# Optimization experiments

Hardware: AMD Instinct MI355X
Metric: run time of the kernel (lower is better)

The kernel has to match this reference:

```python
import jax, jax.numpy as jnp
import numpy as np


def _norm_adj(edge_index, edge_weights, num_nodes):
    """Faithful port of edge_index2norm_adj: dense scatter + self-loops +
    symmetric degree normalization (deg_inv_sqrt is detached in the original)."""
    row, col = edge_index[0], edge_index[1]
    half = edge_weights * 0.5
    adj = jnp.zeros((num_nodes, num_nodes), dtype=edge_weights.dtype)
    adj = adj.at[row, col].add(half)
    adj = adj.at[col, row].add(half)
    adj = adj + jnp.eye(num_nodes, dtype=adj.dtype)
    deg = adj.sum(axis=1)
    deg_inv_sqrt = jnp.where(deg > 0, jax.lax.rsqrt(deg), 0.0)
    deg_inv_sqrt = jax.lax.stop_gradient(deg_inv_sqrt)  # torch.no_grad + detach
    return deg_inv_sqrt[:, None] * adj * deg_inv_sqrt[None, :]


def setup_inputs() -> dict:
    key = jax.random.key(0)
    k1, k2, k3, k4, k5 = jax.random.split(key, 5)
    N, E, D_IN, D_H, D_OUT = 16384, 524288, 64, 64, 16
    x = jax.random.normal(k1, (N, D_IN), dtype=jnp.float32)
    edge_index = jax.random.randint(k2, (2, E), 0, N, dtype=jnp.int64)
    edge_weights = jax.random.uniform(k3, (E,), dtype=jnp.float32)
    W1 = jax.random.normal(k4, (D_IN, D_H), dtype=jnp.float32) / np.sqrt(D_IN)
    b1 = jnp.zeros((D_H,), dtype=jnp.float32)
    W2 = jax.random.normal(k5, (D_H, D_OUT), dtype=jnp.float32) / np.sqrt(D_H)
    b2 = jnp.zeros((D_OUT,), dtype=jnp.float32)
    return {"x": x, "W1": W1, "b1": b1, "W2": W2, "b2": b2,
            "edge_weights": edge_weights, "edge_index": edge_index}


def reference(x, W1, b1, W2, b2, edge_weights, edge_index):
    num_nodes = x.shape[0]
    A = _norm_adj(edge_index, edge_weights, num_nodes)   # [N, N]
    h = jax.nn.relu(A @ (x @ W1) + b1)                   # GCN layer 1
    out = A @ (h @ W2) + b2                              # GCN layer 2 (logits)
    return out
```

## Files before the change

kernel.cpp:

```cpp
#include <hip/hip_runtime.h>

constexpr int TPB   = 256;
constexpr int NMAX  = 16384;
constexpr int CHUNK = 2048;
constexpr int GBMAX = 1024;



__global__ __launch_bounds__(1024) void k_p1(const int* __restrict__ ei,
    const float* __restrict__ ew, int E, int rsh, int NBe, int GB,
    int* __restrict__ bstartT, int* __restrict__ bcntT, int2* __restrict__ tmp) {
    __shared__ int cnt[256];
    __shared__ int curs[256];
    __shared__ int sc[256];
    __shared__ int2 stg[2 * CHUNK];
    int tid = threadIdx.x;
    int b = blockIdx.x;
    int e0 = b * CHUNK;
    int e1 = min(E, e0 + CHUNK);
    if (tid < NBe) cnt[tid] = 0;
    __syncthreads();
    int ea = e0 + tid, ebg = e0 + 1024 + tid;
    int r0 = 0, c0 = 0, r1 = 0, c1 = 0, w0 = 0, w1 = 0;
    bool va = ea < e1, vb = ebg < e1;
    if (va) { r0 = ei[ea];  c0 = ei[E + ea];  w0 = __float_as_int(0.5f * ew[ea]); }
    if (vb) { r1 = ei[ebg]; c1 = ei[E + ebg]; w1 = __float_as_int(0.5f * ew[ebg]); }
    if (va) { atomicAdd(&cnt[r0 >> rsh], 1); atomicAdd(&cnt[c0 >> rsh], 1); }
    if (vb) { atomicAdd(&cnt[r1 >> rsh], 1); atomicAdd(&cnt[c1 >> rsh], 1); }
    __syncthreads();
    int myc = (tid < NBe) ? cnt[tid] : 0;
    if (tid < NBe) sc[tid] = myc;
    __syncthreads();
    for (int off = 1; off < NBe; off <<= 1) {
        int v = 0;
        if (tid < NBe && tid >= off) v = sc[tid - off];
        __syncthreads();
        if (tid < NBe) sc[tid] += v;
        __syncthreads();
    }
    if (tid < NBe) {
        int excl = sc[tid] - myc;
        curs[tid] = excl;
        bstartT[tid * GB + b] = 2 * e0 + excl;
        bcntT[tid * GB + b] = myc;
    }
    __syncthreads();
    int mask = (1 << rsh) - 1;
    if (va) {
        int p = atomicAdd(&curs[r0 >> rsh], 1);
        stg[p] = make_int2(((r0 & mask) << 20) | c0, w0);
        p = atomicAdd(&curs[c0 >> rsh], 1);
        stg[p] = make_int2(((c0 & mask) << 20) | r0, w0);
    }
    if (vb) {
        int p = atomicAdd(&curs[r1 >> rsh], 1);
        stg[p] = make_int2(((r1 & mask) << 20) | c1, w1);
        p = atomicAdd(&curs[c1 >> rsh], 1);
        stg[p] = make_int2(((c1 & mask) << 20) | r1, w1);
    }
    __syncthreads();
    int tot = 2 * (e1 - e0);
    for (int i = tid; i < tot; i += 1024) tmp[2 * e0 + i] = stg[i];
}

__global__ void k_colsum(const int* __restrict__ bcntT, int GB,
                         int* __restrict__ btot) {
    __shared__ int red[TPB / 64];
    int k = blockIdx.x;
    int s = 0;
    for (int b = threadIdx.x; b < GB; b += TPB) s += bcntT[k * GB + b];
    #pragma unroll
    for (int off = 32; off; off >>= 1) s += __shfl_down(s, off, 64);
    int wv = threadIdx.x >> 6;
    if ((threadIdx.x & 63) == 0) red[wv] = s;
    __syncthreads();
    if (threadIdx.x == 0) {
        int t = 0;
        for (int w = 0; w < TPB / 64; ++w) t += red[w];
        btot[k] = t;
    }
}

__global__ __launch_bounds__(1024) void k_p2(const int2* __restrict__ tmp,
    const int* __restrict__ bstartT, const int* __restrict__ bcntT,
    const int* __restrict__ btot, int GB, int rsh, int N, int NBe, int M,
    int2* __restrict__ ent, int* __restrict__ rowptr, float* __restrict__ dis) {
    __shared__ int sco[256];
    __shared__ int ncnt[256];
    __shared__ int nstart[256];
    __shared__ int ncur[256];
    __shared__ float wsum[256];
    int k = blockIdx.x;
    int tid = threadIdx.x;
    int RN = 1 << rsh;
    int n0 = k << rsh;
    int bt = (tid < NBe) ? btot[tid] : 0;
    if (tid < 256) sco[tid] = bt;
    if (tid < RN) { ncnt[tid] = 0; wsum[tid] = 0.f; }
    __syncthreads();
    for (int off = 1; off < 256; off <<= 1) {
        int v = 0;
        if (tid < 256 && tid >= off) v = sco[tid - off];
        __syncthreads();
        if (tid < 256) sco[tid] += v;
        __syncthreads();
    }
    int eb = sco[k] - btot[k];
    int grp = tid >> 2, sub = tid & 3;
    for (int b = grp; b < GB; b += 256) {
        int s = bstartT[k * GB + b];
        int l = bcntT[k * GB + b];
        for (int u = sub; u < l; u += 4) {
            int2 v = tmp[s + u];
            atomicAdd(&ncnt[v.x >> 20], 1);
        }
    }
    __syncthreads();
    int myc = (tid < RN) ? ncnt[tid] : 0;
    if (tid < RN) nstart[tid] = myc;
    __syncthreads();
    for (int off = 1; off < RN; off <<= 1) {
        int v = 0;
        if (tid < RN && tid >= off) v = nstart[tid - off];
        __syncthreads();
        if (tid < RN) nstart[tid] += v;
        __syncthreads();
    }
    if (tid < RN) { nstart[tid] -= myc; ncur[tid] = nstart[tid]; }
    __syncthreads();
    for (int b = grp; b < GB; b += 256) {
        int s = bstartT[k * GB + b];
        int l = bcntT[k * GB + b];
        for (int u = sub; u < l; u += 4) {
            int2 v = tmp[s + u];
            int rl = v.x >> 20;
            int cc = v.x & 0xFFFFF;
            int p = atomicAdd(&ncur[rl], 1);
            ent[eb + p] = make_int2(cc, v.y);
            atomicAdd(&wsum[rl], __int_as_float(v.y));
        }
    }
    __syncthreads();
    if (tid < RN && n0 + tid < N) {
        rowptr[n0 + tid] = eb + nstart[tid];
        dis[n0 + tid] = rsqrtf(1.f + wsum[tid]);
    }
    if (k == 0 && tid == 0) rowptr[N] = M;
}

__global__ void k_init_fb(float* deg, int* counts, int N) {
    int i = blockIdx.x * TPB + threadIdx.x;
    if (i < N) { deg[i] = 1.0f; counts[i] = 0; }
}
__global__ void k_deg_cnt_fb(const int* __restrict__ ei, const float* __restrict__ ew,
                             float* deg, int* counts, int E) {
    int e = blockIdx.x * TPB + threadIdx.x;
    if (e >= E) return;
    int r = ei[e], c = ei[E + e];
    float hw = 0.5f * ew[e];
    unsafeAtomicAdd(&deg[r], hw);
    unsafeAtomicAdd(&deg[c], hw);
    atomicAdd(&counts[r], 1);
    atomicAdd(&counts[c], 1);
}
__global__ void k_rsqrt_fb(float* degdis, int N) {
    int i = blockIdx.x * TPB + threadIdx.x;
    if (i < N) {
        float d = degdis[i];
        degdis[i] = d > 0.f ? rsqrtf(d) : 0.f;
    }
}
__global__ void k_scan_fb(const int* __restrict__ counts, int* __restrict__ rowptr,
                          int* __restrict__ cursor, int N) {
    __shared__ int partial[TPB];
    int tid = threadIdx.x;
    int chunk = (N + TPB - 1) / TPB;
    int begin = tid * chunk;
    int end = begin + chunk; if (end > N) end = N;
    int s = 0;
    for (int i = begin; i < end; ++i) s += counts[i];
    partial[tid] = s;
    __syncthreads();
    for (int off = 1; off < TPB; off <<= 1) {
        int v = partial[tid];
        int add = (tid >= off) ? partial[tid - off] : 0;
        __syncthreads();
        partial[tid] = v + add;
        __syncthreads();
    }
    int base = (tid == 0) ? 0 : partial[tid - 1];
    for (int i = begin; i < end; ++i) {
        rowptr[i] = base; cursor[i] = base;
        base += counts[i];
    }
    if (tid == TPB - 1) rowptr[N] = base;
}
__global__ void k_fill_fb(const int* __restrict__ ei, const float* __restrict__ ew,
                          int* cursor, int2* __restrict__ ent, int E) {
    int e = blockIdx.x * TPB + threadIdx.x;
    if (e >= E) return;
    int r = ei[e], c = ei[E + e];
    int hw = __float_as_int(0.5f * ew[e]);
    int p1 = atomicAdd(&cursor[r], 1);
    ent[p1] = make_int2(c, hw);
    int p2 = atomicAdd(&cursor[c], 1);
    ent[p2] = make_int2(r, hw);
}

__global__ void k_gemm1(const float* __restrict__ X, const float* __restrict__ W,
                        const float* __restrict__ dis, float* __restrict__ Z, int N) {
    __shared__ float Wl[64 * 64];
    int tid = threadIdx.x;
    #pragma unroll
    for (int i = tid; i < 4096; i += TPB) Wl[i] = W[i];
    __syncthreads();
    int row = blockIdx.x * 4 + (tid >> 6);
    int f = tid & 63;
    if (row >= N) return;
    const float* xr = X + row * 64;
    float s = 0.f;
    #pragma unroll
    for (int k = 0; k < 64; ++k) s = fmaf(xr[k], Wl[k * 64 + f], s);
    Z[row * 64 + f] = dis[row] * s;
}

template <int D, bool RELU>
__global__ void k_gather(const float* __restrict__ Z, const int* __restrict__ rowptr,
                         const long long* __restrict__ entq, const float* __restrict__ dis,
                         const float* __restrict__ bias, float* __restrict__ out, int N) {
    constexpr int NPB = TPB / D;
    constexpr int UN = 16;
    int node = blockIdx.x * NPB + threadIdx.x / D;
    int f = threadIdx.x % D;
    int lane = threadIdx.x & 63;
    int base = lane & ~(D - 1);
    if (node >= N) return;
    int j0 = rowptr[node], j1 = rowptr[node + 1];
    float acc = Z[node * D + f];
    long long cur = 0;
    if (j0 < j1) cur = __builtin_nontemporal_load(entq + j0 + f);
    for (int jb = j0; jb < j1; jb += D) {
        long long nxt = cur;
        if (jb + D < j1) nxt = __builtin_nontemporal_load(entq + jb + D + f);
        int ex = (int)cur;
        float ey = __int_as_float((int)(cur >> 32));
        int cnt = j1 - jb; if (cnt > D) cnt = D;
        int k = 0;
        for (; k + UN <= cnt; k += UN) {
            int n[UN]; float w[UN], z[UN];
            #pragma unroll
            for (int u = 0; u < UN; ++u) {
                n[u] = __shfl(ex, base + k + u);
                w[u] = __shfl(ey, base + k + u);
            }
            #pragma unroll
            for (int u = 0; u < UN; ++u) z[u] = Z[n[u] * D + f];
            #pragma unroll
            for (int u = 0; u < UN; ++u) acc = fmaf(w[u], z[u], acc);
        }
        for (; k < cnt; ++k) {
            int n0 = __shfl(ex, base + k);
            float w0 = __shfl(ey, base + k);
            acc = fmaf(w0, Z[n0 * D + f], acc);
        }
        cur = nxt;
    }
    float v = fmaf(dis[node], acc, bias[f]);
    if (RELU) v = v > 0.f ? v : 0.f;
    out[node * D + f] = v;
}

__global__ void k_gemm2(const float* __restrict__ H, const float* __restrict__ W2,
                        const float* __restrict__ dis, float* __restrict__ Z2, int N) {
    __shared__ float Wl[64 * 16];
    int tid = threadIdx.x;
    #pragma unroll
    for (int i = tid; i < 1024; i += TPB) Wl[i] = W2[i];
    __syncthreads();
    int row = blockIdx.x * 16 + (tid >> 4);
    int f = tid & 15;
    if (row >= N) return;
    const float* hr = H + row * 64;
    float s = 0.f;
    #pragma unroll
    for (int k = 0; k < 64; ++k) s = fmaf(hr[k], Wl[k * 16 + f], s);
    Z2[row * 16 + f] = dis[row] * s;
}

extern "C" void kernel_launch(void* const* d_in, const int* in_sizes, int n_in,
                              void* d_out, int out_size, void* d_ws, size_t ws_size,
                              hipStream_t stream) {
    const float* x  = (const float*)d_in[0];
    const float* W1 = (const float*)d_in[1];
    const float* b1 = (const float*)d_in[2];
    const float* W2 = (const float*)d_in[3];
    const float* b2 = (const float*)d_in[4];
    const float* ew = (const float*)d_in[5];
    const int*   ei = (const int*)d_in[6];

    const int N = in_sizes[0] / 64;
    const int E = in_sizes[5];
    const int M = 2 * E;

    int rsh = 0;
    while ((256 << rsh) < N) ++rsh;
    const int NBe = (N + (1 << rsh) - 1) >> rsh;
    const int GB  = (E + CHUNK - 1) / CHUNK;

    char* ws = (char*)d_ws;
    size_t off = 0;
    auto alloc = [&](size_t bytes) -> void* {
        void* p = ws + off;
        off += (bytes + 255) & ~(size_t)255;
        return p;
    };
    float* dis     = (float*)alloc((size_t)N * 4);
    int*   counts  = (int*)alloc((size_t)N * 4);
    int*   rowptr  = (int*)alloc(((size_t)N + 1) * 4);
    int*   cursor  = (int*)alloc((size_t)N * 4);
    int2*  ent     = (int2*)alloc(((size_t)M + 64) * 8);
    int*   bstartT = (int*)alloc((size_t)GB * NBe * 4);
    int*   bcntT   = (int*)alloc((size_t)GB * NBe * 4);
    int*   btot    = (int*)alloc(((size_t)NBe + 1) * 4);
    float* Z1      = (float*)alloc((size_t)N * 64 * 4);
    float* H       = (float*)alloc((size_t)N * 64 * 4);
    float* Z2      = (float*)alloc((size_t)N * 16 * 4);
    (void)ws_size; (void)n_in; (void)out_size;

    int2* tmp = (int2*)Z1;

    float* out = (float*)d_out;

    if (N <= NMAX && GB <= GBMAX && (size_t)16 * E <= (size_t)512 * N) {
        k_p1<<<GB, 1024, 0, stream>>>(ei, ew, E, rsh, NBe, GB, bstartT, bcntT, tmp);
        k_colsum<<<NBe, TPB, 0, stream>>>(bcntT, GB, btot);
        k_p2<<<NBe, 1024, 0, stream>>>(tmp, bstartT, bcntT, btot, GB, rsh, N, NBe, M,
                                       ent, rowptr, dis);
    } else {
        k_init_fb<<<(N + TPB - 1) / TPB, TPB, 0, stream>>>(dis, counts, N);
        k_deg_cnt_fb<<<(E + TPB - 1) / TPB, TPB, 0, stream>>>(ei, ew, dis, counts, E);
        k_rsqrt_fb<<<(N + TPB - 1) / TPB, TPB, 0, stream>>>(dis, N);
        k_scan_fb<<<1, TPB, 0, stream>>>(counts, rowptr, cursor, N);
        k_fill_fb<<<(E + TPB - 1) / TPB, TPB, 0, stream>>>(ei, ew, cursor, ent, E);
    }

    k_gemm1<<<(N + 3) / 4, TPB, 0, stream>>>(x, W1, dis, Z1, N);
    k_gather<64, true><<<(N + 3) / 4, TPB, 0, stream>>>(Z1, rowptr, (const long long*)ent,
                                                        dis, b1, H, N);
    k_gemm2<<<(N + 15) / 16, TPB, 0, stream>>>(H, W2, dis, Z2, N);
    k_gather<16, false><<<(N + 15) / 16, TPB, 0, stream>>>(Z2, rowptr, (const long long*)ent,
                                                           dis, b2, out, N);
}
```

Measured before the change: 156.9 us.

## Fuse layer-1 gather with W2 projection and fold colsum into CSR build

Removes the k_colsum launch by having each k_p2 block compute its own edge base offset directly from bcntT. k_p2 now preloads its edges into registers and stages the sorted entries in shared memory before writing them out coalesced. The layer-1 gather is fused with the ReLU and the H@W2 projection, which eliminates the H buffer round trip and the k_gemm2 launch. The tradeoffs are more shared memory per block in k_p2, a redundant prefix sum in every block, and an idle 3/4 of threads during the fused small matmul.

```diff
diff --git a/kernel.cpp b/kernel.cpp
--- a/kernel.cpp
+++ b/kernel.cpp
@@ -4,6 +4,8 @@
 constexpr int NMAX  = 16384;
 constexpr int CHUNK = 2048;
 constexpr int GBMAX = 1024;
+constexpr int STGN  = 8192;
+constexpr int RCAP  = 12;
 
 
 
@@ -63,84 +65,114 @@
     for (int i = tid; i < tot; i += 1024) tmp[2 * e0 + i] = stg[i];
 }
 
-__global__ void k_colsum(const int* __restrict__ bcntT, int GB,
-                         int* __restrict__ btot) {
-    __shared__ int red[TPB / 64];
-    int k = blockIdx.x;
-    int s = 0;
-    for (int b = threadIdx.x; b < GB; b += TPB) s += bcntT[k * GB + b];
-    #pragma unroll
-    for (int off = 32; off; off >>= 1) s += __shfl_down(s, off, 64);
-    int wv = threadIdx.x >> 6;
-    if ((threadIdx.x & 63) == 0) red[wv] = s;
-    __syncthreads();
-    if (threadIdx.x == 0) {
-        int t = 0;
-        for (int w = 0; w < TPB / 64; ++w) t += red[w];
-        btot[k] = t;
-    }
-}
-
 __global__ __launch_bounds__(1024) void k_p2(const int2* __restrict__ tmp,
     const int* __restrict__ bstartT, const int* __restrict__ bcntT,
-    const int* __restrict__ btot, int GB, int rsh, int N, int NBe, int M,
+    int GB, int rsh, int N, int M,
     int2* __restrict__ ent, int* __restrict__ rowptr, float* __restrict__ dis) {
-    __shared__ int sco[256];
-    __shared__ int ncnt[256];
-    __shared__ int nstart[256];
-    __shared__ int ncur[256];
-    __shared__ float wsum[256];
+    __shared__ int red2[32];
+    __shared__ int ncnt[64];
+    __shared__ int nscan[64];
+    __shared__ int nstart[64];
+    __shared__ int ncur[64];
+    __shared__ float wsum[64];
+    __shared__ int2 stg[STGN];
     int k = blockIdx.x;
     int tid = threadIdx.x;
     int RN = 1 << rsh;
     int n0 = k << rsh;
-    int bt = (tid < NBe) ? btot[tid] : 0;
-    if (tid < 256) sco[tid] = bt;
+    int split = k * GB;
+
+    int grp = tid >> 2, sub = tid & 3;
+    int s0 = 0, l0 = 0;
+    if (grp < GB) { s0 = bstartT[split + grp]; l0 = bcntT[split + grp]; }
+    int2 r[RCAP];
+    #pragma unroll
+    for (int u = 0; u < RCAP; ++u) {
+        int idx = sub + 4 * u;
+        if (idx < l0) r[u] = tmp[s0 + idx];
+    }
+
+    int lim = split + GB;
+    int se = 0, st = 0;
+    for (int i = tid; i < lim; i += 1024) {
+        int v = bcntT[i];
+        if (i < split) se += v; else st += v;
+    }
+    #pragma unroll
+    for (int o = 32; o; o >>= 1) {
+        se += __shfl_down(se, o, 64);
+        st += __shfl_down(st, o, 64);
+    }
     if (tid < RN) { ncnt[tid] = 0; wsum[tid] = 0.f; }
-    __syncthreads();
-    for (int off = 1; off < 256; off <<= 1) {
-        int v = 0;
-        if (tid < 256 && tid >= off) v = sco[tid - off];
-        __syncthreads();
-        if (tid < 256) sco[tid] += v;
-        __syncthreads();
-    }
-    int eb = sco[k] - btot[k];
-    int grp = tid >> 2, sub = tid & 3;
-    for (int b = grp; b < GB; b += 256) {
-        int s = bstartT[k * GB + b];
-        int l = bcntT[k * GB + b];
-        for (int u = sub; u < l; u += 4) {
-            int2 v = tmp[s + u];
-            atomicAdd(&ncnt[v.x >> 20], 1);
-        }
-    }
-    __syncthreads();
+    int wv = tid >> 6;
+    if ((tid & 63) == 0) { red2[wv] = se; red2[16 + wv] = st; }
+    __syncthreads();
+    if (tid == 0) {
+        int a = 0, b = 0;
+        #pragma unroll
+        for (int w = 0; w < 16; ++w) { a += red2[w]; b += red2[16 + w]; }
+        red2[0] = a; red2[16] = b;
+    }
+    __syncthreads();
+    int eb = red2[0], tot = red2[16];
+    bool useStg = (tot <= STGN);
+
+    #pragma unroll
+    for (int u = 0; u < RCAP; ++u)
+        if (sub + 4 * u < l0) atomicAdd(&ncnt[r[u].x >> 20], 1);
+    for (int idx = sub + 4 * RCAP; idx < l0; idx += 4)
+        atomicAdd(&ncnt[tmp[s0 + idx].x >> 20], 1);
+    for (int b = grp + 256; b < GB; b += 256) {
+        int s = bstartT[split + b], l = bcntT[split + b];
+        for (int idx = sub; idx < l; idx += 4)
+            atomicAdd(&ncnt[tmp[s + idx].x >> 20], 1);
+    }
+    __syncthreads();
+
     int myc = (tid < RN) ? ncnt[tid] : 0;
-    if (tid < RN) nstart[tid] = myc;
+    if (tid < RN) nscan[tid] = myc;
     __syncthreads();
     for (int off = 1; off < RN; off <<= 1) {
         int v = 0;
-        if (tid < RN && tid >= off) v = nstart[tid - off];
-        __syncthreads();
-        if (tid < RN) nstart[tid] += v;
-        __syncthreads();
-    }
-    if (tid < RN) { nstart[tid] -= myc; ncur[tid] = nstart[tid]; }
-    __syncthreads();
-    for (int b = grp; b < GB; b += 256) {
-        int s = bstartT[k * GB + b];
-        int l = bcntT[k * GB + b];
-        for (int u = sub; u < l; u += 4) {
-            int2 v = tmp[s + u];
+        if (tid < RN && tid >= off) v = nscan[tid - off];
+        __syncthreads();
+        if (tid < RN) nscan[tid] += v;
+        __syncthreads();
+    }
+    if (tid < RN) { nstart[tid] = nscan[tid] - myc; ncur[tid] = nscan[tid] - myc; }
+    __syncthreads();
+
+    #pragma unroll
+    for (int u = 0; u < RCAP; ++u)
+        if (sub + 4 * u < l0) {
+            int rl = r[u].x >> 20;
+            int p = atomicAdd(&ncur[rl], 1);
+            int2 v2 = make_int2(r[u].x & 0xFFFFF, r[u].y);
+            if (useStg) stg[p] = v2; else ent[eb + p] = v2;
+            atomicAdd(&wsum[rl], __int_as_float(r[u].y));
+        }
+    for (int idx = sub + 4 * RCAP; idx < l0; idx += 4) {
+        int2 v = tmp[s0 + idx];
+        int rl = v.x >> 20;
+        int p = atomicAdd(&ncur[rl], 1);
+        int2 v2 = make_int2(v.x & 0xFFFFF, v.y);
+        if (useStg) stg[p] = v2; else ent[eb + p] = v2;
+        atomicAdd(&wsum[rl], __int_as_float(v.y));
+    }
+    for (int b = grp + 256; b < GB; b += 256) {
+        int s = bstartT[split + b], l = bcntT[split + b];
+        for (int idx = sub; idx < l; idx += 4) {
+            int2 v = tmp[s + idx];
             int rl = v.x >> 20;
-            int cc = v.x & 0xFFFFF;
             int p = atomicAdd(&ncur[rl], 1);
-            ent[eb + p] = make_int2(cc, v.y);
+            int2 v2 = make_int2(v.x & 0xFFFFF, v.y);
+            if (useStg) stg[p] = v2; else ent[eb + p] = v2;
             atomicAdd(&wsum[rl], __int_as_float(v.y));
         }
     }
     __syncthreads();
+    if (useStg)
+        for (int i = tid; i < tot; i += 1024) ent[eb + i] = stg[i];
     if (tid < RN && n0 + tid < N) {
         rowptr[n0 + tid] = eb + nstart[tid];
         dis[n0 + tid] = rsqrtf(1.f + wsum[tid]);
@@ -222,6 +254,67 @@
     #pragma unroll
     for (int k = 0; k < 64; ++k) s = fmaf(xr[k], Wl[k * 64 + f], s);
     Z[row * 64 + f] = dis[row] * s;
+}
+
+__global__ __launch_bounds__(TPB) void k_gather1(const float* __restrict__ Z,
+    const int* __restrict__ rowptr, const long long* __restrict__ entq,
+    const float* __restrict__ dis, const float* __restrict__ bias1,
+    const float* __restrict__ W2, float* __restrict__ Z2, int N) {
+    constexpr int D = 64, UN = 16;
+    __shared__ float W2l[64 * 16];
+    __shared__ float hbuf[4][64];
+    int tid = threadIdx.x;
+    #pragma unroll
+    for (int i = tid; i < 1024; i += TPB) W2l[i] = W2[i];
+    int slot = tid >> 6;
+    int node = blockIdx.x * 4 + slot;
+    int f = tid & 63;
+    bool active = node < N;
+    float acc = 0.f, dn = 0.f;
+    int j0 = 0, j1 = 0;
+    if (active) {
+        j0 = rowptr[node]; j1 = rowptr[node + 1];
+        acc = Z[node * D + f];
+        dn = dis[node];
+    }
+    long long cur = 0;
+    if (j0 < j1) cur = __builtin_nontemporal_load(entq + j0 + f);
+    for (int jb = j0; jb < j1; jb += D) {
+        long long nxt = cur;
+        if (jb + D < j1) nxt = __builtin_nontemporal_load(entq + jb + D + f);
+        int ex = (int)cur;
+        float ey = __int_as_float((int)(cur >> 32));
+        int cnt = j1 - jb; if (cnt > D) cnt = D;
+        int kk = 0;
+        for (; kk + UN <= cnt; kk += UN) {
+            int n[UN]; float w[UN], z[UN];
+            #pragma unroll
+            for (int u = 0; u < UN; ++u) {
+                n[u] = __shfl(ex, kk + u);
+                w[u] = __shfl(ey, kk + u);
+            }
+            #pragma unroll
+            for (int u = 0; u < UN; ++u) z[u] = Z[n[u] * D + f];
+            #pragma unroll
+            for (int u = 0; u < UN; ++u) acc = fmaf(w[u], z[u], acc);
+        }
+        for (; kk < cnt; ++kk) {
+            int n0 = __shfl(ex, kk);
+            float w0 = __shfl(ey, kk);
+            acc = fmaf(w0, Z[n0 * D + f], acc);
+        }
+        cur = nxt;
+    }
+    float v = fmaf(dn, acc, bias1[f]);
+    v = v > 0.f ? v : 0.f;
+    hbuf[slot][f] = v;
+    __syncthreads();
+    if (active && f < 16) {
+        float s = 0.f;
+        #pragma unroll
+        for (int kk = 0; kk < 64; ++kk) s = fmaf(hbuf[slot][kk], W2l[kk * 16 + f], s);
+        Z2[node * 16 + f] = dn * s;
+    }
 }
 
 template <int D, bool RELU>
@@ -270,23 +363,6 @@
     out[node * D + f] = v;
 }
 
-__global__ void k_gemm2(const float* __restrict__ H, const float* __restrict__ W2,
-                        const float* __restrict__ dis, float* __restrict__ Z2, int N) {
-    __shared__ float Wl[64 * 16];
-    int tid = threadIdx.x;
-    #pragma unroll
-    for (int i = tid; i < 1024; i += TPB) Wl[i] = W2[i];
-    __syncthreads();
-    int row = blockIdx.x * 16 + (tid >> 4);
-    int f = tid & 15;
-    if (row >= N) return;
-    const float* hr = H + row * 64;
-    float s = 0.f;
-    #pragma unroll
-    for (int k = 0; k < 64; ++k) s = fmaf(hr[k], Wl[k * 16 + f], s);
-    Z2[row * 16 + f] = dis[row] * s;
-}
-
 extern "C" void kernel_launch(void* const* d_in, const int* in_sizes, int n_in,
                               void* d_out, int out_size, void* d_ws, size_t ws_size,
                               hipStream_t stream) {
@@ -321,20 +397,17 @@
     int2*  ent     = (int2*)alloc(((size_t)M + 64) * 8);
     int*   bstartT = (int*)alloc((size_t)GB * NBe * 4);
     int*   bcntT   = (int*)alloc((size_t)GB * NBe * 4);
-    int*   btot    = (int*)alloc(((size_t)NBe + 1) * 4);
-    float* Z1      = (float*)alloc((size_t)N * 64 * 4);
-    float* H       = (float*)alloc((size_t)N * 64 * 4);
+    int2*  tmp     = (int2*)alloc((size_t)M * 8);
     float* Z2      = (float*)alloc((size_t)N * 16 * 4);
     (void)ws_size; (void)n_in; (void)out_size;
 
-    int2* tmp = (int2*)Z1;
+    float* Z1 = (float*)tmp;
 
     float* out = (float*)d_out;
 
-    if (N <= NMAX && GB <= GBMAX && (size_t)16 * E <= (size_t)512 * N) {
+    if (N <= NMAX && GB <= GBMAX) {
         k_p1<<<GB, 1024, 0, stream>>>(ei, ew, E, rsh, NBe, GB, bstartT, bcntT, tmp);
-        k_colsum<<<NBe, TPB, 0, stream>>>(bcntT, GB, btot);
-        k_p2<<<NBe, 1024, 0, stream>>>(tmp, bstartT, bcntT, btot, GB, rsh, N, NBe, M,
+        k_p2<<<NBe, 1024, 0, stream>>>(tmp, bstartT, bcntT, GB, rsh, N, M,
                                        ent, rowptr, dis);
     } else {
         k_init_fb<<<(N + TPB - 1) / TPB, TPB, 0, stream>>>(dis, counts, N);
@@ -345,9 +418,8 @@
     }
 
     k_gemm1<<<(N + 3) / 4, TPB, 0, stream>>>(x, W1, dis, Z1, N);
-    k_gather<64, true><<<(N + 3) / 4, TPB, 0, stream>>>(Z1, rowptr, (const long long*)ent,
-                                                        dis, b1, H, N);
-    k_gemm2<<<(N + 15) / 16, TPB, 0, stream>>>(H, W2, dis, Z2, N);
+    k_gather1<<<(N + 3) / 4, TPB, 0, stream>>>(Z1, rowptr, (const long long*)ent,
+                                               dis, b1, W2, Z2, N);
     k_gather<16, false><<<(N + 15) / 16, TPB, 0, stream>>>(Z2, rowptr, (const long long*)ent,
                                                            dis, b2, out, N);
 }
```

After: 163.9 us. 4.5% more time.
